# Kernel tuning notes

Hardware: AMD Instinct MI355X
Metric: run time of the kernel (lower is better)

## Reference

```python
import jax, jax.numpy as jnp
import numpy as np

B, D, LEAVES, MID = 131072, 256, 4, 2


def setup_inputs() -> dict:
    key = jax.random.key(0)
    ks = jax.random.split(key, 5)
    s = 1.0 / np.sqrt(D).astype(np.float32)
    return {
        "x": jax.random.normal(ks[0], (B, D), jnp.float32),
        "Wg": jax.random.normal(ks[1], (D, LEAVES), jnp.float32) * s,
        "bg": jnp.zeros((LEAVES,), jnp.float32),
        "W_leaf": jax.random.normal(ks[2], (LEAVES, D, D), jnp.float32) * s,
        "b_leaf": jnp.zeros((LEAVES, D), jnp.float32),
        "W_mid": jax.random.normal(ks[3], (MID, D, D), jnp.float32) * s,
        "b_mid": jnp.zeros((MID, D), jnp.float32),
        "W_root": jax.random.normal(ks[4], (D, D), jnp.float32) * s,
        "b_root": jnp.zeros((D,), jnp.float32),
    }


def reference(x, Wg, bg, W_leaf, b_leaf, W_mid, b_mid, W_root, b_root):
    # Gate: argmax over leaf experts (torch.max(...).indices over dim=1)
    logits = x @ Wg + bg                      # [B, LEAVES]
    idx = jnp.argmax(logits, axis=1)          # [B] leaf expert per sample
    pidx = idx // 2                           # [B] parent (mid-level) node on the path

    # Leaf level: compute all 4 leaf experts (small E), select routed one.
    h1_all = jax.nn.relu(jnp.einsum('bd,edh->beh', x, W_leaf) + b_leaf)   # [B,4,D]
    h1 = jnp.take_along_axis(h1_all, idx[:, None, None], axis=1)[:, 0]    # [B,D]

    # Mid level: the parent of the selected leaf.
    h2_all = jax.nn.relu(jnp.einsum('bd,pdh->bph', h1, W_mid) + b_mid)    # [B,2,D]
    h2 = jnp.take_along_axis(h2_all, pidx[:, None, None], axis=1)[:, 0]   # [B,D]

    # Root (shared by all paths). end is None -> returned directly.
    return jax.nn.relu(h2 @ W_root + b_root)                              # [B,D]
```

## Files before the change

kernel.cpp:

```cpp
#include <hip/hip_runtime.h>
#include <hip/hip_bf16.h>
#include <stdint.h>

#define B_ROWS 131072
#define DDIM 256
#define TILES_PER_EXPERT 2048

typedef short bf16x8 __attribute__((ext_vector_type(8)));
typedef float f32x4 __attribute__((ext_vector_type(4)));

__device__ __forceinline__ unsigned short f32_to_bf16_rne(float f) {
    union { float f; uint32_t u; } v; v.f = f;
    uint32_t u = v.u;
    u += 0x7fffu + ((u >> 16) & 1u);
    return (unsigned short)(u >> 16);
}

__global__ __launch_bounds__(256) void prepack_weights(
    const float* __restrict__ Wl, const float* __restrict__ Wm,
    const float* __restrict__ Wr, unsigned short* __restrict__ out)
{
    int o = blockIdx.x * 256 + threadIdx.x;
    int m = o >> 16;
    int w = o & 65535;
    int j = w & 7;
    int l = (w >> 3) & 63;
    int t = (w >> 9) & 15;
    int s = w >> 13;
    int k = 32 * s + 8 * (l >> 4) + j;
    int n = 16 * t + (l & 15);
    const float* src = (m < 4) ? (Wl + m * 65536)
                     : (m < 6) ? (Wm + (m - 4) * 65536)
                               : Wr;
    out[o] = f32_to_bf16_rne(src[k * 256 + n]);
}

__global__ __launch_bounds__(256) void gate_kernel(
    const float* __restrict__ x, const float* __restrict__ Wg,
    const float* __restrict__ bg, int* __restrict__ counts,
    int* __restrict__ perm)
{
    __shared__ float wgl[1024];
    __shared__ int hcount[4];
    __shared__ int hbase[4];

    int t = threadIdx.x;
    ((float4*)wgl)[t] = ((const float4*)Wg)[t];
    if (t < 4) hcount[t] = 0;
    __syncthreads();

    int lrow = t >> 2, sub = t & 3;
    int row = blockIdx.x * 64 + lrow;
    const float* xr = x + (long)row * DDIM;

    double a0 = 0.0, a1 = 0.0, a2 = 0.0, a3 = 0.0;
    #pragma unroll
    for (int i = 0; i < 16; i++) {
        int k0 = i * 16 + sub * 4;
        float4 v = *(const float4*)(xr + k0);
        #pragma unroll
        for (int kk = 0; kk < 4; kk++) {
            float xv = (kk == 0) ? v.x : (kk == 1) ? v.y : (kk == 2) ? v.z : v.w;
            const float* wr = wgl + (k0 + kk) * 4;
            a0 += (double)xv * (double)wr[0];
            a1 += (double)xv * (double)wr[1];
            a2 += (double)xv * (double)wr[2];
            a3 += (double)xv * (double)wr[3];
        }
    }
    a0 += __shfl_xor(a0, 1); a0 += __shfl_xor(a0, 2);
    a1 += __shfl_xor(a1, 1); a1 += __shfl_xor(a1, 2);
    a2 += __shfl_xor(a2, 1); a2 += __shfl_xor(a2, 2);
    a3 += __shfl_xor(a3, 1); a3 += __shfl_xor(a3, 2);

    int myidx = 0, mylpos = 0;
    if (sub == 0) {
        double l0 = a0 + (double)bg[0];
        double l1 = a1 + (double)bg[1];
        double l2 = a2 + (double)bg[2];
        double l3 = a3 + (double)bg[3];
        double best = l0; myidx = 0;
        if (l1 > best) { best = l1; myidx = 1; }
        if (l2 > best) { best = l2; myidx = 2; }
        if (l3 > best) { best = l3; myidx = 3; }
        mylpos = atomicAdd(&hcount[myidx], 1);
    }
    __syncthreads();
    if (t < 4) hbase[t] = atomicAdd(&counts[t], hcount[t]);
    __syncthreads();
    if (sub == 0) perm[myidx * B_ROWS + hbase[myidx] + mylpos] = row;
}

__device__ __forceinline__ void run_level(
    const unsigned short* __restrict__ wp, const float* __restrict__ bias_g,
    unsigned short* apack, f32x4 acc[4][4], float bias[4], int wv, int l)
{
    #pragma unroll
    for (int nt = 0; nt < 4; nt++)
        bias[nt] = bias_g[(4 * wv + nt) * 16 + (l & 15)];
    f32x4 z = {0.f, 0.f, 0.f, 0.f};
    #pragma unroll
    for (int mt = 0; mt < 4; mt++)
        #pragma unroll
        for (int nt = 0; nt < 4; nt++) acc[mt][nt] = z;

    const bf16x8* wpv = (const bf16x8*)wp;
    #pragma unroll
    for (int s = 0; s < 8; s++) {
        bf16x8 a[4], b[4];
        const bf16x8* ap = (const bf16x8*)(apack + s * 4 * 64 * 8);
        #pragma unroll
        for (int mt = 0; mt < 4; mt++) a[mt] = ap[mt * 64 + l];
        #pragma unroll
        for (int nt = 0; nt < 4; nt++) b[nt] = wpv[(s * 16 + 4 * wv + nt) * 64 + l];
        #pragma unroll
        for (int mt = 0; mt < 4; mt++)
            #pragma unroll
            for (int nt = 0; nt < 4; nt++)
                acc[mt][nt] = __builtin_amdgcn_mfma_f32_16x16x32_bf16(
                    a[mt], b[nt], acc[mt][nt], 0, 0, 0);
    }
}

__device__ __forceinline__ void epilogue_lds(
    unsigned short* apack, f32x4 acc[4][4], float bias[4], int wv, int l)
{
    #pragma unroll
    for (int nt = 0; nt < 4; nt++) {
        int col = (4 * wv + nt) * 16 + (l & 15);
        int s = col >> 5;
        int fq = (col >> 3) & 3;
        int j = col & 7;
        #pragma unroll
        for (int mt = 0; mt < 4; mt++) {
            #pragma unroll
            for (int r = 0; r < 4; r++) {
                float v = fmaxf(acc[mt][nt][r] + bias[nt], 0.f);
                int row_l = ((l >> 4) << 2) + r;
                int fl = row_l + 16 * fq;
                apack[((s * 4 + mt) * 64 + fl) * 8 + j] = f32_to_bf16_rne(v);
            }
        }
    }
}

__global__ __launch_bounds__(256, 2) void mlp_kernel(
    const float* __restrict__ x, const unsigned short* __restrict__ wpack,
    const float* __restrict__ b_leaf, const float* __restrict__ b_mid,
    const float* __restrict__ b_root, const int* __restrict__ counts,
    const int* __restrict__ perm, float* __restrict__ out)
{
    __shared__ unsigned short apack[16384];
    __shared__ int rowsLds[64];

    int e = blockIdx.x >> 11;
    int tile = blockIdx.x & 2047;
    int cnt = counts[e];
    int base = tile * 64;
    if (base >= cnt) return;

    int t = threadIdx.x;
    if (t < 64) {
        int src = base + t;
        if (src >= cnt) src = base;
        rowsLds[t] = perm[e * B_ROWS + src];
    }
    __syncthreads();

    {
        int lrow = t >> 2, sub = t & 3;
        const float* xr = x + (long)rowsLds[lrow] * DDIM;
        int mt = lrow >> 4;
        int rl = lrow & 15;
        #pragma unroll
        for (int i = 0; i < 16; i++) {
            int k0 = i * 16 + sub * 4;
            float4 v = *(const float4*)(xr + k0);
            int s = k0 >> 5;
            int fl = rl + 16 * ((k0 >> 3) & 3);
            ushort4 u;
            u.x = f32_to_bf16_rne(v.x);
            u.y = f32_to_bf16_rne(v.y);
            u.z = f32_to_bf16_rne(v.z);
            u.w = f32_to_bf16_rne(v.w);
            *(ushort4*)&apack[((s * 4 + mt) * 64 + fl) * 8 + (k0 & 7)] = u;
        }
    }
    __syncthreads();

    int wv = t >> 6, l = t & 63;
    f32x4 acc[4][4];
    float bias[4];

    run_level(wpack + e * 65536, b_leaf + e * 256, apack, acc, bias, wv, l);
    __syncthreads();
    epilogue_lds(apack, acc, bias, wv, l);
    __syncthreads();

    run_level(wpack + (4 + (e >> 1)) * 65536, b_mid + (e >> 1) * 256, apack, acc, bias, wv, l);
    __syncthreads();
    epilogue_lds(apack, acc, bias, wv, l);
    __syncthreads();

    run_level(wpack + 6 * 65536, b_root, apack, acc, bias, wv, l);
    #pragma unroll
    for (int nt = 0; nt < 4; nt++) {
        int col = (4 * wv + nt) * 16 + (l & 15);
        #pragma unroll
        for (int mt = 0; mt < 4; mt++) {
            #pragma unroll
            for (int r = 0; r < 4; r++) {
                int row_local = mt * 16 + ((l >> 4) << 2) + r;
                if (base + row_local < cnt) {
                    long grow = rowsLds[row_local];
                    out[grow * DDIM + col] = fmaxf(acc[mt][nt][r] + bias[nt], 0.f);
                }
            }
        }
    }
}

extern "C" void kernel_launch(void* const* d_in, const int* in_sizes, int n_in,
                              void* d_out, int out_size, void* d_ws, size_t ws_size,
                              hipStream_t stream) {
    const float* x      = (const float*)d_in[0];
    const float* Wg     = (const float*)d_in[1];
    const float* bg     = (const float*)d_in[2];
    const float* W_leaf = (const float*)d_in[3];
    const float* b_leaf = (const float*)d_in[4];
    const float* W_mid  = (const float*)d_in[5];
    const float* b_mid  = (const float*)d_in[6];
    const float* W_root = (const float*)d_in[7];
    const float* b_root = (const float*)d_in[8];
    float* out = (float*)d_out;

    char* ws = (char*)d_ws;
    int* counts = (int*)ws;
    int* perm = (int*)(ws + 256);
    unsigned short* wpack = (unsigned short*)(ws + (4 << 20));

    hipMemsetAsync(counts, 0, 16, stream);
    prepack_weights<<<1792, 256, 0, stream>>>(W_leaf, W_mid, W_root, wpack);
    gate_kernel<<<B_ROWS / 64, 256, 0, stream>>>(x, Wg, bg, counts, perm);
    mlp_kernel<<<4 * TILES_PER_EXPERT, 256, 0, stream>>>(
        x, wpack, b_leaf, b_mid, b_root, counts, perm, out);
}
```

Baseline: 360.8 us.

## Double MLP row tile to 128 and fuse gate with coalesced weight prepack

The MLP tile grows from 64 to 128 rows per block, so each weight fragment loaded from global memory is reused across 8 M-tiles instead of 4. This halves the number of weight reads per row but doubles the accumulator registers and the LDS footprint, which may cut occupancy. The gate and weight-prepack kernels are merged into one launch to save a launch. The prepack now stages through LDS so that global reads and writes are coalesced float4/uint4 accesses.

```diff
diff --git a/kernel.cpp b/kernel.cpp
--- a/kernel.cpp
+++ b/kernel.cpp
@@ -4,7 +4,9 @@
 
 #define B_ROWS 131072
 #define DDIM 256
-#define TILES_PER_EXPERT 2048
+#define GATE_BLOCKS 2048
+#define PREPACK_BLOCKS 56
+#define TILES_PER_EXPERT 1024
 
 typedef short bf16x8 __attribute__((ext_vector_type(8)));
 typedef float f32x4 __attribute__((ext_vector_type(4)));
@@ -16,35 +18,50 @@
     return (unsigned short)(u >> 16);
 }
 
-__global__ __launch_bounds__(256) void prepack_weights(
-    const float* __restrict__ Wl, const float* __restrict__ Wm,
-    const float* __restrict__ Wr, unsigned short* __restrict__ out)
+__global__ __launch_bounds__(256) void gate_prepack_kernel(
+    const float* __restrict__ x, const float* __restrict__ Wg,
+    const float* __restrict__ bg, const float* __restrict__ Wl,
+    const float* __restrict__ Wm, const float* __restrict__ Wr,
+    int* __restrict__ counts, int* __restrict__ perm,
+    unsigned short* __restrict__ wpack)
 {
-    int o = blockIdx.x * 256 + threadIdx.x;
-    int m = o >> 16;
-    int w = o & 65535;
-    int j = w & 7;
-    int l = (w >> 3) & 63;
-    int t = (w >> 9) & 15;
-    int s = w >> 13;
-    int k = 32 * s + 8 * (l >> 4) + j;
-    int n = 16 * t + (l & 15);
-    const float* src = (m < 4) ? (Wl + m * 65536)
-                     : (m < 6) ? (Wm + (m - 4) * 65536)
-                               : Wr;
-    out[o] = f32_to_bf16_rne(src[k * 256 + n]);
-}
-
-__global__ __launch_bounds__(256) void gate_kernel(
-    const float* __restrict__ x, const float* __restrict__ Wg,
-    const float* __restrict__ bg, int* __restrict__ counts,
-    int* __restrict__ perm)
-{
-    __shared__ float wgl[1024];
-    __shared__ int hcount[4];
-    __shared__ int hbase[4];
-
+    __shared__ float smemf[4160];
     int t = threadIdx.x;
+
+    if (blockIdx.x >= GATE_BLOCKS) {
+        int bid = blockIdx.x - GATE_BLOCKS;
+        int m = bid >> 3, s = bid & 7;
+        const float* src = (m < 4) ? (Wl + m * 65536)
+                         : (m < 6) ? (Wm + (m - 4) * 65536)
+                                   : Wr;
+        unsigned short* lds = (unsigned short*)smemf;
+        #pragma unroll
+        for (int i = 0; i < 8; i++) {
+            int v = i * 256 + t;
+            int kp = v >> 6;
+            int n0 = (v & 63) * 4;
+            float4 w = *(const float4*)(src + (32 * s + kp) * 256 + n0);
+            #pragma unroll
+            for (int c = 0; c < 4; c++) {
+                int n = n0 + c;
+                float val = (c == 0) ? w.x : (c == 1) ? w.y : (c == 2) ? w.z : w.w;
+                int o = (n >> 4) * 512 + ((n & 15) + 16 * (kp >> 3)) * 8 + (kp & 7);
+                lds[o] = f32_to_bf16_rne(val);
+            }
+        }
+        __syncthreads();
+        uint4* outv = (uint4*)(wpack + (m * 8 + s) * 8192);
+        const uint4* ldsv = (const uint4*)lds;
+        #pragma unroll
+        for (int q = 0; q < 4; q++)
+            outv[q * 256 + t] = ldsv[q * 256 + t];
+        return;
+    }
+
+    float* wgl = smemf;
+    int* hcount = (int*)(smemf + 1024);
+    int* hbase  = (int*)(smemf + 1028);
+
     ((float4*)wgl)[t] = ((const float4*)Wg)[t];
     if (t < 4) hcount[t] = 0;
     __syncthreads();
@@ -61,11 +78,11 @@
         #pragma unroll
         for (int kk = 0; kk < 4; kk++) {
             float xv = (kk == 0) ? v.x : (kk == 1) ? v.y : (kk == 2) ? v.z : v.w;
-            const float* wr = wgl + (k0 + kk) * 4;
-            a0 += (double)xv * (double)wr[0];
-            a1 += (double)xv * (double)wr[1];
-            a2 += (double)xv * (double)wr[2];
-            a3 += (double)xv * (double)wr[3];
+            float4 w = *(const float4*)(wgl + (k0 + kk) * 4);
+            a0 += (double)xv * (double)w.x;
+            a1 += (double)xv * (double)w.y;
+            a2 += (double)xv * (double)w.z;
+            a3 += (double)xv * (double)w.w;
         }
     }
     a0 += __shfl_xor(a0, 1); a0 += __shfl_xor(a0, 2);
@@ -91,76 +108,23 @@
     if (sub == 0) perm[myidx * B_ROWS + hbase[myidx] + mylpos] = row;
 }
 
-__device__ __forceinline__ void run_level(
-    const unsigned short* __restrict__ wp, const float* __restrict__ bias_g,
-    unsigned short* apack, f32x4 acc[4][4], float bias[4], int wv, int l)
-{
-    #pragma unroll
-    for (int nt = 0; nt < 4; nt++)
-        bias[nt] = bias_g[(4 * wv + nt) * 16 + (l & 15)];
-    f32x4 z = {0.f, 0.f, 0.f, 0.f};
-    #pragma unroll
-    for (int mt = 0; mt < 4; mt++)
-        #pragma unroll
-        for (int nt = 0; nt < 4; nt++) acc[mt][nt] = z;
-
-    const bf16x8* wpv = (const bf16x8*)wp;
-    #pragma unroll
-    for (int s = 0; s < 8; s++) {
-        bf16x8 a[4], b[4];
-        const bf16x8* ap = (const bf16x8*)(apack + s * 4 * 64 * 8);
-        #pragma unroll
-        for (int mt = 0; mt < 4; mt++) a[mt] = ap[mt * 64 + l];
-        #pragma unroll
-        for (int nt = 0; nt < 4; nt++) b[nt] = wpv[(s * 16 + 4 * wv + nt) * 64 + l];
-        #pragma unroll
-        for (int mt = 0; mt < 4; mt++)
-            #pragma unroll
-            for (int nt = 0; nt < 4; nt++)
-                acc[mt][nt] = __builtin_amdgcn_mfma_f32_16x16x32_bf16(
-                    a[mt], b[nt], acc[mt][nt], 0, 0, 0);
-    }
-}
-
-__device__ __forceinline__ void epilogue_lds(
-    unsigned short* apack, f32x4 acc[4][4], float bias[4], int wv, int l)
-{
-    #pragma unroll
-    for (int nt = 0; nt < 4; nt++) {
-        int col = (4 * wv + nt) * 16 + (l & 15);
-        int s = col >> 5;
-        int fq = (col >> 3) & 3;
-        int j = col & 7;
-        #pragma unroll
-        for (int mt = 0; mt < 4; mt++) {
-            #pragma unroll
-            for (int r = 0; r < 4; r++) {
-                float v = fmaxf(acc[mt][nt][r] + bias[nt], 0.f);
-                int row_l = ((l >> 4) << 2) + r;
-                int fl = row_l + 16 * fq;
-                apack[((s * 4 + mt) * 64 + fl) * 8 + j] = f32_to_bf16_rne(v);
-            }
-        }
-    }
-}
-
 __global__ __launch_bounds__(256, 2) void mlp_kernel(
     const float* __restrict__ x, const unsigned short* __restrict__ wpack,
     const float* __restrict__ b_leaf, const float* __restrict__ b_mid,
     const float* __restrict__ b_root, const int* __restrict__ counts,
     const int* __restrict__ perm, float* __restrict__ out)
 {
-    __shared__ unsigned short apack[16384];
-    __shared__ int rowsLds[64];
-
-    int e = blockIdx.x >> 11;
-    int tile = blockIdx.x & 2047;
+    __shared__ unsigned short apack[32768];
+    __shared__ int rowsLds[128];
+
+    int e = blockIdx.x >> 10;
+    int tile = blockIdx.x & 1023;
     int cnt = counts[e];
-    int base = tile * 64;
+    int base = tile * 128;
     if (base >= cnt) return;
 
     int t = threadIdx.x;
-    if (t < 64) {
+    if (t < 128) {
         int src = base + t;
         if (src >= cnt) src = base;
         rowsLds[t] = perm[e * B_ROWS + src];
@@ -168,13 +132,12 @@
     __syncthreads();
 
     {
-        int lrow = t >> 2, sub = t & 3;
-        const float* xr = x + (long)rowsLds[lrow] * DDIM;
-        int mt = lrow >> 4;
-        int rl = lrow & 15;
-        #pragma unroll
-        for (int i = 0; i < 16; i++) {
-            int k0 = i * 16 + sub * 4;
+        int r = t >> 1, sub = t & 1;
+        const float* xr = x + (long)rowsLds[r] * DDIM;
+        int mt = r >> 4, rl = r & 15;
+        #pragma unroll
+        for (int i = 0; i < 32; i++) {
+            int k0 = sub * 128 + i * 4;
             float4 v = *(const float4*)(xr + k0);
             int s = k0 >> 5;
             int fl = rl + 16 * ((k0 >> 3) & 3);
@@ -183,31 +146,79 @@
             u.y = f32_to_bf16_rne(v.y);
             u.z = f32_to_bf16_rne(v.z);
             u.w = f32_to_bf16_rne(v.w);
-            *(ushort4*)&apack[((s * 4 + mt) * 64 + fl) * 8 + (k0 & 7)] = u;
+            *(ushort4*)&apack[((s * 8 + mt) * 64 + fl) * 8 + (k0 & 7)] = u;
         }
     }
     __syncthreads();
 
     int wv = t >> 6, l = t & 63;
-    f32x4 acc[4][4];
+    f32x4 acc[8][4];
     float bias[4];
 
-    run_level(wpack + e * 65536, b_leaf + e * 256, apack, acc, bias, wv, l);
-    __syncthreads();
-    epilogue_lds(apack, acc, bias, wv, l);
-    __syncthreads();
-
-    run_level(wpack + (4 + (e >> 1)) * 65536, b_mid + (e >> 1) * 256, apack, acc, bias, wv, l);
-    __syncthreads();
-    epilogue_lds(apack, acc, bias, wv, l);
-    __syncthreads();
-
-    run_level(wpack + 6 * 65536, b_root, apack, acc, bias, wv, l);
+    auto run_level = [&](const unsigned short* wp, const float* bias_g) {
+        #pragma unroll
+        for (int nt = 0; nt < 4; nt++)
+            bias[nt] = bias_g[(4 * wv + nt) * 16 + (l & 15)];
+        f32x4 z = {0.f, 0.f, 0.f, 0.f};
+        #pragma unroll
+        for (int mt = 0; mt < 8; mt++)
+            #pragma unroll
+            for (int nt = 0; nt < 4; nt++) acc[mt][nt] = z;
+
+        const bf16x8* wpv = (const bf16x8*)wp;
+        #pragma unroll
+        for (int s = 0; s < 8; s++) {
+            bf16x8 b[4];
+            #pragma unroll
+            for (int nt = 0; nt < 4; nt++)
+                b[nt] = wpv[(s * 16 + 4 * wv + nt) * 64 + l];
+            const bf16x8* ap = (const bf16x8*)(apack + s * 8 * 64 * 8);
+            #pragma unroll
+            for (int mt = 0; mt < 8; mt++) {
+                bf16x8 a = ap[mt * 64 + l];
+                #pragma unroll
+                for (int nt = 0; nt < 4; nt++)
+                    acc[mt][nt] = __builtin_amdgcn_mfma_f32_16x16x32_bf16(
+                        a, b[nt], acc[mt][nt], 0, 0, 0);
+            }
+        }
+    };
+
+    auto epilogue_lds = [&]() {
+        #pragma unroll
+        for (int nt = 0; nt < 4; nt++) {
+            int col = (4 * wv + nt) * 16 + (l & 15);
+            int s = col >> 5;
+            int fq = (col >> 3) & 3;
+            int j = col & 7;
+            #pragma unroll
+            for (int mt = 0; mt < 8; mt++) {
+                #pragma unroll
+                for (int r = 0; r < 4; r++) {
+                    float v = fmaxf(acc[mt][nt][r] + bias[nt], 0.f);
+                    int fl = ((l >> 4) << 2) + r + 16 * fq;
+                    apack[((s * 8 + mt) * 64 + fl) * 8 + j] = f32_to_bf16_rne(v);
+                }
+            }
+        }
+    };
+
+    run_level(wpack + e * 65536, b_leaf + e * 256);
+    __syncthreads();
+    epilogue_lds();
+    __syncthreads();
+
+    run_level(wpack + (4 + (e >> 1)) * 65536, b_mid + (e >> 1) * 256);
+    __syncthreads();
+    epilogue_lds();
+    __syncthreads();
+
+    run_level(wpack + 6 * 65536, b_root);
     #pragma unroll
     for (int nt = 0; nt < 4; nt++) {
         int col = (4 * wv + nt) * 16 + (l & 15);
         #pragma unroll
-        for (int mt = 0; mt < 4; mt++) {
+        for (int mt = 0; mt < 8; mt++) {
             #pragma unroll
             for (int r = 0; r < 4; r++) {
                 int row_local = mt * 16 + ((l >> 4) << 2) + r;
@@ -240,8 +251,8 @@
     unsigned short* wpack = (unsigned short*)(ws + (4 << 20));
 
     hipMemsetAsync(counts, 0, 16, stream);
-    prepack_weights<<<1792, 256, 0, stream>>>(W_leaf, W_mid, W_root, wpack);
-    gate_kernel<<<B_ROWS / 64, 256, 0, stream>>>(x, Wg, bg, counts, perm);
+    gate_prepack_kernel<<<GATE_BLOCKS + PREPACK_BLOCKS, 256, 0, stream>>>(
+        x, Wg, bg, W_leaf, W_mid, W_root, counts, perm, wpack);
     mlp_kernel<<<4 * TILES_PER_EXPERT, 256, 0, stream>>>(
         x, wpack, b_leaf, b_mid, b_root, counts, perm, out);
 }
```

After: 368.1 us. 2.0% more time.
